# Optimization experiments

Hardware: AMD Instinct MI355X
Metric: run time of the kernel (lower is better)

The kernel has to match this reference:

```python
import jax, jax.numpy as jnp
import numpy as np

B, L, E, H, K = 256, 500, 300, 10, 5  # batch, doc_len, word_embedding, h1, num_aspects


def setup_inputs() -> dict:
    key = jax.random.key(0)
    k1, k2, k3 = jax.random.split(key, 3)
    review = jax.random.normal(k1, (B, L, E), dtype=jnp.float32)
    # params initialized uniform(-0.01, 0.01) as in the torch module
    aspProj = jax.random.uniform(k2, (K, E, H), dtype=jnp.float32, minval=-0.01, maxval=0.01)
    aspEmbed = jax.random.uniform(k3, (K, 3 * H), dtype=jnp.float32, minval=-0.01, maxval=0.01)
    return {"review": review, "aspProj": aspProj, "aspEmbed": aspEmbed}


def reference(review, aspProj, aspEmbed):
    # project review into each aspect subspace: (K, B, L, H)
    proj = jnp.einsum('ble,keh->kblh', review, aspProj)
    # pad seq dim by 1 on each side, build window-3 unfold.
    # torch unfold(1,3,1) yields (B, L, H, 3) then reshape to (B, L, 3*H),
    # i.e. feature layout is (h_index, window_offset) -- match by stacking
    # window offsets on the LAST axis before the reshape.
    padded = jnp.pad(proj, ((0, 0), (0, 0), (1, 1), (0, 0)))
    windows = jnp.stack([padded[:, :, i:i + L, :] for i in range(3)], axis=-1)  # (K,B,L,H,3)
    windows = windows.reshape(K, windows.shape[1], L, 3 * H)  # (K,B,L,3H)
    # attention logits per position, softmax over the WHOLE sequence dim
    scores = jnp.einsum('kblf,kf->kbl', windows, aspEmbed)
    attn = jax.nn.softmax(scores, axis=-1)  # (K,B,L)
    # attention-weighted sum over sequence -> aspect representation
    rep = jnp.einsum('kblh,kbl->kbh', proj, attn)  # (K,B,H)
    batch_aspAttn = jnp.transpose(attn, (1, 0, 2))  # (B,K,L)
    batch_aspRep = jnp.transpose(rep, (1, 0, 2))    # (B,K,H)
    return (batch_aspAttn, batch_aspRep)
```

## Files before the change

kernel.cpp:

```cpp
#include <hip/hip_runtime.h>

#define BB 256
#define LL 500
#define EE 300
#define HH 10
#define KK 5
#define NF 50
#define NT 512
#define NWAVE 8

#define MP 512
#define CK 32
#define NCH 10
#define BP 328
#define PP 53
#define NA4 3750

#define B_BYTES  (64 * BP * 2)
#define PROJ_OFF B_BYTES
#define RED_OFF  (PROJ_OFF + MP * PP * 4)
#define REP_OFF  (RED_OFF + KK * NWAVE * 4)
#define EMB_OFF  (REP_OFF + NWAVE * NF * 4)
#define SMEM_BYTES (EMB_OFF + KK * 3 * HH * 4)

typedef __attribute__((ext_vector_type(8))) short short8;
typedef __attribute__((ext_vector_type(4))) float f32x4;

__device__ __forceinline__ unsigned int f2bf(float x) {
    unsigned int u = __float_as_uint(x);
    return (u + 0x7FFFu + ((u >> 16) & 1u)) >> 16;
}

__device__ __forceinline__ short8 pack8(float4 a, float4 b) {
    short8 r;
    r[0] = (short)f2bf(a.x); r[1] = (short)f2bf(a.y);
    r[2] = (short)f2bf(a.z); r[3] = (short)f2bf(a.w);
    r[4] = (short)f2bf(b.x); r[5] = (short)f2bf(b.y);
    r[6] = (short)f2bf(b.z); r[7] = (short)f2bf(b.w);
    return r;
}

__global__ __launch_bounds__(NT, 2) void anr_mfma4(
    const float* __restrict__ review,
    const float* __restrict__ aspProj,
    const float* __restrict__ aspEmbed,
    float* __restrict__ out)
{
    __shared__ __align__(16) char smem[SMEM_BYTES];
    short* B16   = (short*)smem;
    float* s_d   = (float*)smem;
    float* proj  = (float*)(smem + PROJ_OFF);
    float* s_red = (float*)(smem + RED_OFF);
    float* s_rep = (float*)(smem + REP_OFF);
    float* s_emb = (float*)(smem + EMB_OFF);

    const int tid  = threadIdx.x;
    const int b    = blockIdx.x;
    const int lane = tid & 63;
    const int w    = tid >> 6;
    const int quad = lane >> 4;
    const int m16  = lane & 15;

    for (int j = tid; j < B_BYTES / 4; j += NT)
        ((int*)smem)[j] = 0;

    const float4* ap4 = (const float4*)aspProj;
    float4 bt[8];
#pragma unroll
    for (int i = 0; i < 8; ++i) {
        int idx = tid + NT * i;
        bt[i] = ap4[(idx < NA4) ? idx : (NA4 - 1)];
    }
    float embv = aspEmbed[(tid < KK * 3 * HH) ? tid : 0];

    const float* revb = review + (size_t)b * LL * EE;
    const float* ar[4];
#pragma unroll
    for (int mi = 0; mi < 4; ++mi) {
        int r = w * 64 + mi * 16 + m16;
        ar[mi] = revb + (size_t)((r < LL) ? r : (LL - 1)) * EE + quad * 8;
    }
    float4 fc[4][2], fn[4][2];
#pragma unroll
    for (int mi = 0; mi < 4; ++mi) {
        fc[mi][0] = *(const float4*)(ar[mi] + 0);
        fc[mi][1] = *(const float4*)(ar[mi] + 4);
    }

    __syncthreads();

#pragma unroll
    for (int i = 0; i < 8; ++i) {
        int idx = tid + NT * i;
        if (idx < NA4) {
            float vv[4] = {bt[i].x, bt[i].y, bt[i].z, bt[i].w};
#pragma unroll
            for (int cm = 0; cm < 4; ++cm) {
                int jj   = 4 * idx + cm;
                int kasp = jj / (EE * HH);
                int rr   = jj - kasp * (EE * HH);
                int e    = rr / HH;
                int h    = rr - e * HH;
                B16[(kasp * HH + h) * BP + e] = (short)f2bf(vv[cm]);
            }
        }
    }
    if (tid < KK * 3 * HH) s_emb[tid] = embv;
    __syncthreads();

    f32x4 acc[4][4];
#pragma unroll
    for (int mi = 0; mi < 4; ++mi)
#pragma unroll
        for (int ni = 0; ni < 4; ++ni)
            acc[mi][ni] = (f32x4){0.f, 0.f, 0.f, 0.f};

#pragma unroll
    for (int c = 0; c < NCH - 1; ++c) {
        if (c < NCH - 2) {
#pragma unroll
            for (int mi = 0; mi < 4; ++mi) {
                fn[mi][0] = *(const float4*)(ar[mi] + (c + 1) * CK);
                fn[mi][1] = *(const float4*)(ar[mi] + (c + 1) * CK + 4);
            }
        } else {
            const float4 z4 = {0.f, 0.f, 0.f, 0.f};
#pragma unroll
            for (int mi = 0; mi < 4; ++mi) {
                fn[mi][0] = (quad < 2) ? *(const float4*)(ar[mi] + (NCH - 1) * CK) : z4;
                fn[mi][1] = (quad < 1) ? *(const float4*)(ar[mi] + (NCH - 1) * CK + 4) : z4;
            }
        }
        short8 bf[4], af[4];
#pragma unroll
        for (int ni = 0; ni < 4; ++ni)
            bf[ni] = *(const short8*)&B16[(ni * 16 + m16) * BP + c * CK + quad * 8];
#pragma unroll
        for (int mi = 0; mi < 4; ++mi)
            af[mi] = pack8(fc[mi][0], fc[mi][1]);
#pragma unroll
        for (int mi = 0; mi < 4; ++mi)
#pragma unroll
            for (int ni = 0; ni < 4; ++ni)
                acc[mi][ni] = __builtin_amdgcn_mfma_f32_16x16x32_bf16(
                    af[mi], bf[ni], acc[mi][ni], 0, 0, 0);
#pragma unroll
        for (int mi = 0; mi < 4; ++mi) {
            fc[mi][0] = fn[mi][0];
            fc[mi][1] = fn[mi][1];
        }
    }
    {
        const int c = NCH - 1;
        short8 bf[4], af[4];
#pragma unroll
        for (int ni = 0; ni < 4; ++ni)
            bf[ni] = *(const short8*)&B16[(ni * 16 + m16) * BP + c * CK + quad * 8];
#pragma unroll
        for (int mi = 0; mi < 4; ++mi)
            af[mi] = pack8(fc[mi][0], fc[mi][1]);
#pragma unroll
        for (int mi = 0; mi < 4; ++mi)
#pragma unroll
            for (int ni = 0; ni < 4; ++ni)
                acc[mi][ni] = __builtin_amdgcn_mfma_f32_16x16x32_bf16(
                    af[mi], bf[ni], acc[mi][ni], 0, 0, 0);
    }

#pragma unroll
    for (int mi = 0; mi < 4; ++mi) {
#pragma unroll
        for (int ni = 0; ni < 4; ++ni) {
            int col = ni * 16 + m16;
            if (col < NF) {
                int row = w * 64 + mi * 16 + quad * 4;
#pragma unroll
                for (int r = 0; r < 4; ++r)
                    proj[(row + r) * PP + col] = acc[mi][ni][r];
            }
        }
    }
    __syncthreads();

    const int l  = tid;
    const bool vl = (l < LL);

    float pr[NF];
#pragma unroll
    for (int f = 0; f < NF; ++f) pr[f] = proj[l * PP + f];

    float d0[KK], d1[KK], d2[KK];
#pragma unroll
    for (int k = 0; k < KK; ++k) {
        float a0 = 0.f, a1 = 0.f, a2 = 0.f;
#pragma unroll
        for (int h = 0; h < HH; ++h) {
            float x = pr[k * HH + h];
            a0 = fmaf(x, s_emb[k * 3 * HH + 3 * h + 0], a0);
            a1 = fmaf(x, s_emb[k * 3 * HH + 3 * h + 1], a1);
            a2 = fmaf(x, s_emb[k * 3 * HH + 3 * h + 2], a2);
        }
        d0[k] = vl ? a0 : 0.f;
        d1[k] = vl ? a1 : 0.f;
        d2[k] = vl ? a2 : 0.f;
    }
#pragma unroll
    for (int k = 0; k < KK; ++k) {
        s_d[(0 * KK + k) * MP + l] = d0[k];
        s_d[(1 * KK + k) * MP + l] = d1[k];
        s_d[(2 * KK + k) * MP + l] = d2[k];
    }
    __syncthreads();

    const int lp1 = (l + 1 < MP) ? l + 1 : MP - 1;
    float sc[KK];
#pragma unroll
    for (int k = 0; k < KK; ++k) {
        float t0 = (l >= 1) ? s_d[(0 * KK + k) * MP + l - 1] : 0.f;
        float t1 = s_d[(1 * KK + k) * MP + l];
        float t2 = s_d[(2 * KK + k) * MP + lp1];
        sc[k] = vl ? (t0 + t1 + t2) : -1e30f;
    }

    float mx[KK];
#pragma unroll
    for (int k = 0; k < KK; ++k) {
        float m = sc[k];
        for (int s = 32; s > 0; s >>= 1) m = fmaxf(m, __shfl_xor(m, s, 64));
        if (lane == 0) s_red[k * NWAVE + w] = m;
    }
    __syncthreads();
#pragma unroll
    for (int k = 0; k < KK; ++k) {
        float m = s_red[k * NWAVE + 0];
#pragma unroll
        for (int ww = 1; ww < NWAVE; ++ww) m = fmaxf(m, s_red[k * NWAVE + ww]);
        mx[k] = m;
    }
    __syncthreads();
    float ex[KK], sm[KK];
#pragma unroll
    for (int k = 0; k < KK; ++k) {
        ex[k] = __expf(sc[k] - mx[k]);
        float s = ex[k];
        for (int sh = 32; sh > 0; sh >>= 1) s += __shfl_xor(s, sh, 64);
        if (lane == 0) s_red[k * NWAVE + w] = s;
    }
    __syncthreads();
#pragma unroll
    for (int k = 0; k < KK; ++k) {
        float s = 0.f;
#pragma unroll
        for (int ww = 0; ww < NWAVE; ++ww) s += s_red[k * NWAVE + ww];
        sm[k] = s;
    }

#pragma unroll
    for (int k = 0; k < KK; ++k) {
        float wk = ex[k] / sm[k];
        if (vl) out[((size_t)b * KK + k) * LL + l] = wk;
#pragma unroll
        for (int h = 0; h < HH; ++h) {
            float v = pr[k * HH + h] * wk;
            for (int sh = 32; sh > 0; sh >>= 1) v += __shfl_xor(v, sh, 64);
            if (lane == 0) s_rep[w * NF + k * HH + h] = v;
        }
    }
    __syncthreads();
    if (tid < NF) {
        float s = 0.f;
#pragma unroll
        for (int ww = 0; ww < NWAVE; ++ww) s += s_rep[ww * NF + tid];
        out[(size_t)BB * KK * LL + (size_t)b * NF + tid] = s;
    }
}

extern "C" void kernel_launch(void* const* d_in, const int* in_sizes, int n_in,
                              void* d_out, int out_size, void* d_ws, size_t ws_size,
                              hipStream_t stream) {
    const float* review   = (const float*)d_in[0];
    const float* aspProj  = (const float*)d_in[1];
    const float* aspEmbed = (const float*)d_in[2];
    float* out = (float*)d_out;

    anr_mfma4<<<dim3(BB), dim3(NT), 0, stream>>>(review, aspProj, aspEmbed, out);
}
```

Baseline: 239.8 us.

## Stream review rows into LDS with async global_load_lds triple buffering

Replaces per-thread register prefetch of review rows with a triple-buffered pipeline. Each wave issues global_load_lds copies of 32-row groups straight into shared memory, two groups ahead of compute. The MFMA work is redistributed so each wave computes one 16x16 tile per group, reading A from LDS, and the proj buffer aliases the staging area. The aim is to overlap HBM streaming with MFMA and keep loads coalesced, at the cost of a barrier per group and much more LDS use, which may lower occupancy.

```diff
diff --git a/kernel.cpp b/kernel.cpp
--- a/kernel.cpp
+++ b/kernel.cpp
@@ -16,11 +16,19 @@
 #define PP 53
 #define NA4 3750
 
-#define B_BYTES  (64 * BP * 2)
-#define PROJ_OFF B_BYTES
-#define RED_OFF  (PROJ_OFF + MP * PP * 4)
-#define REP_OFF  (RED_OFF + KK * NWAVE * 4)
-#define EMB_OFF  (REP_OFF + NWAVE * NF * 4)
+#define NG 16
+#define GROWS 32
+#define G_BYTES (GROWS * EE * 4)
+#define W_BYTES (G_BYTES / NWAVE)
+#define REV_BYTES (LL * EE * 4)
+
+#define B_BYTES   (64 * BP * 2)
+#define STG_OFF   B_BYTES
+#define STG_STRIDE (G_BYTES + 128)
+#define PROJ_OFF  STG_OFF
+#define RED_OFF   (STG_OFF + 3 * STG_STRIDE)
+#define REP_OFF   (RED_OFF + KK * NWAVE * 4)
+#define EMB_OFF   (REP_OFF + NWAVE * NF * 4)
 #define SMEM_BYTES (EMB_OFF + KK * 3 * HH * 4)
 
 typedef __attribute__((ext_vector_type(8))) short short8;
@@ -40,7 +48,25 @@
     return r;
 }
 
-__global__ __launch_bounds__(NT, 2) void anr_mfma4(
+__device__ __forceinline__ void stage_grp(const char* revb, char* smem,
+                                          int g, int w, int lane) {
+    char* ldsb = smem + STG_OFF + (g % 3) * STG_STRIDE + w * W_BYTES;
+    const char* gs = revb + (size_t)g * G_BYTES + (size_t)w * W_BYTES;
+    const char* glim = revb + (REV_BYTES - 16);
+#pragma unroll
+    for (int j = 0; j < 5; ++j) {
+        if (j < 4 || lane < 44) {
+            const char* ga = gs + j * 1024 + lane * 16;
+            if (ga > glim) ga = glim;
+            __builtin_amdgcn_global_load_lds(
+                (const __attribute__((address_space(1))) void*)ga,
+                (__attribute__((address_space(3))) void*)(ldsb + j * 1024),
+                16, 0, 0);
+        }
+    }
+}
+
+__global__ __launch_bounds__(NT, 2) void anr_mfma5(
     const float* __restrict__ review,
     const float* __restrict__ aspProj,
     const float* __restrict__ aspEmbed,
@@ -60,9 +86,7 @@
     const int w    = tid >> 6;
     const int quad = lane >> 4;
     const int m16  = lane & 15;
-
-    for (int j = tid; j < B_BYTES / 4; j += NT)
-        ((int*)smem)[j] = 0;
+    const char* revb = (const char*)(review + (size_t)b * LL * EE);
 
     const float4* ap4 = (const float4*)aspProj;
     float4 bt[8];
@@ -73,21 +97,16 @@
     }
     float embv = aspEmbed[(tid < KK * 3 * HH) ? tid : 0];
 
-    const float* revb = review + (size_t)b * LL * EE;
-    const float* ar[4];
-#pragma unroll
-    for (int mi = 0; mi < 4; ++mi) {
-        int r = w * 64 + mi * 16 + m16;
-        ar[mi] = revb + (size_t)((r < LL) ? r : (LL - 1)) * EE + quad * 8;
-    }
-    float4 fc[4][2], fn[4][2];
-#pragma unroll
-    for (int mi = 0; mi < 4; ++mi) {
-        fc[mi][0] = *(const float4*)(ar[mi] + 0);
-        fc[mi][1] = *(const float4*)(ar[mi] + 4);
-    }
-
-    __syncthreads();
+    for (int j = tid; j < B_BYTES / 4; j += NT)
+        ((int*)smem)[j] = 0;
+    if (tid < 96) {
+        int bi = tid >> 5, wi = tid & 31;
+        ((int*)(smem + STG_OFF + bi * STG_STRIDE + G_BYTES))[wi] = 0;
+    }
+    __syncthreads();
+
+    stage_grp(revb, smem, 0, w, lane);
+    stage_grp(revb, smem, 1, w, lane);
 
 #pragma unroll
     for (int i = 0; i < 8; ++i) {
@@ -106,78 +125,42 @@
         }
     }
     if (tid < KK * 3 * HH) s_emb[tid] = embv;
-    __syncthreads();
-
-    f32x4 acc[4][4];
-#pragma unroll
-    for (int mi = 0; mi < 4; ++mi)
-#pragma unroll
-        for (int ni = 0; ni < 4; ++ni)
-            acc[mi][ni] = (f32x4){0.f, 0.f, 0.f, 0.f};
-
-#pragma unroll
-    for (int c = 0; c < NCH - 1; ++c) {
-        if (c < NCH - 2) {
-#pragma unroll
-            for (int mi = 0; mi < 4; ++mi) {
-                fn[mi][0] = *(const float4*)(ar[mi] + (c + 1) * CK);
-                fn[mi][1] = *(const float4*)(ar[mi] + (c + 1) * CK + 4);
-            }
-        } else {
-            const float4 z4 = {0.f, 0.f, 0.f, 0.f};
-#pragma unroll
-            for (int mi = 0; mi < 4; ++mi) {
-                fn[mi][0] = (quad < 2) ? *(const float4*)(ar[mi] + (NCH - 1) * CK) : z4;
-                fn[mi][1] = (quad < 1) ? *(const float4*)(ar[mi] + (NCH - 1) * CK + 4) : z4;
-            }
-        }
-        short8 bf[4], af[4];
-#pragma unroll
-        for (int ni = 0; ni < 4; ++ni)
-            bf[ni] = *(const short8*)&B16[(ni * 16 + m16) * BP + c * CK + quad * 8];
-#pragma unroll
-        for (int mi = 0; mi < 4; ++mi)
-            af[mi] = pack8(fc[mi][0], fc[mi][1]);
-#pragma unroll
-        for (int mi = 0; mi < 4; ++mi)
-#pragma unroll
-            for (int ni = 0; ni < 4; ++ni)
-                acc[mi][ni] = __builtin_amdgcn_mfma_f32_16x16x32_bf16(
-                    af[mi], bf[ni], acc[mi][ni], 0, 0, 0);
-#pragma unroll
-        for (int mi = 0; mi < 4; ++mi) {
-            fc[mi][0] = fn[mi][0];
-            fc[mi][1] = fn[mi][1];
-        }
-    }
-    {
-        const int c = NCH - 1;
-        short8 bf[4], af[4];
-#pragma unroll
-        for (int ni = 0; ni < 4; ++ni)
-            bf[ni] = *(const short8*)&B16[(ni * 16 + m16) * BP + c * CK + quad * 8];
-#pragma unroll
-        for (int mi = 0; mi < 4; ++mi)
-            af[mi] = pack8(fc[mi][0], fc[mi][1]);
-#pragma unroll
-        for (int mi = 0; mi < 4; ++mi)
-#pragma unroll
-            for (int ni = 0; ni < 4; ++ni)
-                acc[mi][ni] = __builtin_amdgcn_mfma_f32_16x16x32_bf16(
-                    af[mi], bf[ni], acc[mi][ni], 0, 0, 0);
-    }
-
-#pragma unroll
-    for (int mi = 0; mi < 4; ++mi) {
-#pragma unroll
-        for (int ni = 0; ni < 4; ++ni) {
-            int col = ni * 16 + m16;
-            if (col < NF) {
-                int row = w * 64 + mi * 16 + quad * 4;
-#pragma unroll
-                for (int r = 0; r < 4; ++r)
-                    proj[(row + r) * PP + col] = acc[mi][ni][r];
-            }
+    asm volatile("s_waitcnt lgkmcnt(0)" ::: "memory");
+
+    f32x4 acc[NG];
+#pragma unroll
+    for (int g = 0; g < NG; ++g) acc[g] = (f32x4){0.f, 0.f, 0.f, 0.f};
+
+    const int arow_off = ((w >> 2) * 16 + m16) * (EE * 4) + quad * 32;
+    const int brow_off = ((w & 3) * 16 + m16) * BP;
+
+#pragma unroll
+    for (int g = 0; g < NG; ++g) {
+        if (g < NG - 1) asm volatile("s_waitcnt vmcnt(5)" ::: "memory");
+        else            asm volatile("s_waitcnt vmcnt(0)" ::: "memory");
+        __builtin_amdgcn_s_barrier();
+
+        const char* ab = smem + STG_OFF + (g % 3) * STG_STRIDE + arow_off;
+#pragma unroll 2
+        for (int c = 0; c < NCH; ++c) {
+            float4 a0 = *(const float4*)(ab + c * 128);
+            float4 a1 = *(const float4*)(ab + c * 128 + 16);
+            short8 af = pack8(a0, a1);
+            short8 bf = *(const short8*)&B16[brow_off + c * CK + quad * 8];
+            acc[g] = __builtin_amdgcn_mfma_f32_16x16x32_bf16(af, bf, acc[g], 0, 0, 0);
+        }
+        if (g + 2 < NG) stage_grp(revb, smem, g + 2, w, lane);
+    }
+    __syncthreads();
+
+#pragma unroll
+    for (int g = 0; g < NG; ++g) {
+        int col = (w & 3) * 16 + m16;
+        if (col < NF) {
+            int row = g * GROWS + (w >> 2) * 16 + quad * 4;
+#pragma unroll
+            for (int r = 0; r < 4; ++r)
+                proj[(row + r) * PP + col] = acc[g][r];
         }
     }
     __syncthreads();
@@ -283,5 +266,5 @@
     const float* aspEmbed = (const float*)d_in[2];
     float* out = (float*)d_out;
 
-    anr_mfma4<<<dim3(BB), dim3(NT), 0, stream>>>(review, aspProj, aspEmbed, out);
-}
+    anr_mfma5<<<dim3(BB), dim3(NT), 0, stream>>>(review, aspProj, aspEmbed, out);
+}
```

Result: no change. 239.6 us (-0.1%).
